# Optimization experiments

Measured on AMD Instinct MI355X. Metric: run time of the kernel, lower is better.

The kernel has to match this reference:

```python
import jax, jax.numpy as jnp
import numpy as np

B, TQ, TK, D, DV = 8, 2048, 2048, 1024, 1024  # units == TK


def setup_inputs() -> dict:
    key = jax.random.key(0)
    kq, kk, kv, kb = jax.random.split(key, 4)
    q = jax.random.normal(kq, (B, TQ, D), dtype=jnp.float32)
    k = jax.random.normal(kk, (B, D, TK), dtype=jnp.float32)
    v = jax.random.normal(kv, (B, TK, DV), dtype=jnp.float32)
    b = 0.1 * jax.random.normal(kb, (TK,), dtype=jnp.float32)  # bias over key axis (units,)
    return {"q": q, "k": k, "v": v, "b": b}


def reference(q, k, v, b):
    # scores[b,i,j] = tanh(q_i . k_j + b_j)   -- additive-style biased dot scores
    scores = jnp.tanh(jnp.einsum("bqd,bdk->bqk", q, k) + b)  # [B, TQ, TK]
    # softmax over the key axis (axis=1 of the unbatched [TQ,TK] scores)
    weights = jax.nn.softmax(scores, axis=-1)
    # weighted sum of values
    context = jnp.einsum("bqk,bkv->bqv", weights, v)  # [B, TQ, DV]
    return context
```

## Files before the change

### kernel.cpp

```cpp
#include <hip/hip_runtime.h>
#include <hip/hip_bf16.h>
#include <stdint.h>

#define B_  8
#define TQ_ 2048
#define TK_ 2048
#define D_  1024
#define DV_ 1024

typedef __attribute__((ext_vector_type(8))) short  short8;
typedef __attribute__((ext_vector_type(4))) float  floatx4;

__device__ __forceinline__ void async_copy16(const void* g, void* l) {
  __builtin_amdgcn_global_load_lds(
      (const __attribute__((address_space(1))) unsigned int*)g,
      (__attribute__((address_space(3))) unsigned int*)l,
      16, 0, 0);
}

__device__ __forceinline__ ushort f2bf(float f) {
  union { __hip_bfloat16 b; ushort u; } cv;
  cv.b = __float2bfloat16(f);
  return cv.u;
}

__device__ __forceinline__ float bf2f(ushort u) {
  union { ushort u; __hip_bfloat16 b; } cv;
  cv.u = u;
  return __bfloat162float(cv.b);
}


__device__ __forceinline__ void transpose_body(const float* __restrict__ in,
                                               ushort* __restrict__ out,
                                               int R, int C, int r0, int c0,
                                               float (*tile)[65]) {
  const int t = threadIdx.x;
  {
    const int row = t >> 4, col = (t & 15) * 4;
    #pragma unroll
    for (int ro = 0; ro < 4; ro++) {
      const float4 f = *(const float4*)&in[(size_t)(r0 + ro * 16 + row) * C + c0 + col];
      tile[ro * 16 + row][col + 0] = f.x;
      tile[ro * 16 + row][col + 1] = f.y;
      tile[ro * 16 + row][col + 2] = f.z;
      tile[ro * 16 + row][col + 3] = f.w;
    }
  }
  __syncthreads();
  {
    const int c = t >> 4, rg = (t & 15) * 4;
    #pragma unroll
    for (int ro = 0; ro < 4; ro++) {
      const int cc = ro * 16 + c;
      ushort4 o;
      o.x = f2bf(tile[rg + 0][cc]);
      o.y = f2bf(tile[rg + 1][cc]);
      o.z = f2bf(tile[rg + 2][cc]);
      o.w = f2bf(tile[rg + 3][cc]);
      *(ushort4*)&out[(size_t)(c0 + cc) * R + r0 + rg] = o;
    }
  }
}

__global__ void prep(const float* __restrict__ q, const float* __restrict__ k,
                     const float* __restrict__ v, ushort* __restrict__ qb,
                     ushort* __restrict__ ktb, ushort* __restrict__ vtb) {
  __shared__ float tile[64][65];
  const int task = blockIdx.z >> 3;
  const int z    = blockIdx.z & 7;
  if (task == 0) {
    const float4* in  = (const float4*)(q + (size_t)z * TQ_ * D_);
    ushort4*      oup = (ushort4*)(qb + (size_t)z * TQ_ * D_);
    const int i0 = (blockIdx.y * 32 + blockIdx.x) * 1024 + threadIdx.x;
    #pragma unroll
    for (int it = 0; it < 4; it++) {
      const int i = i0 + it * 256;
      float4 f = in[i];
      ushort4 o;
      o.x = f2bf(f.x); o.y = f2bf(f.y); o.z = f2bf(f.z); o.w = f2bf(f.w);
      oup[i] = o;
    }
  } else if (task == 1) {
    transpose_body(k + (size_t)z * D_ * TK_, ktb + (size_t)z * TK_ * D_,
                   D_, TK_, blockIdx.y * 64, blockIdx.x * 64, tile);
  } else {
    transpose_body(v + (size_t)z * TK_ * DV_, vtb + (size_t)z * DV_ * TK_,
                   TK_, DV_, blockIdx.x * 64, blockIdx.y * 64, tile);
  }
}

template <int KDIM>
__device__ __forceinline__ void gemm_core(const ushort* __restrict__ Ab,
                                          const ushort* __restrict__ Bb,
                                          ushort* ldsA, ushort* ldsB,
                                          int bm0, int bn0,
                                          floatx4 (&acc)[4][4]) {
  const int t    = threadIdx.x;
  const int lane = t & 63;
  const int w    = t >> 6;
  const int wm   = w >> 1, wn = w & 1;
  const int lc   = lane & 15;
  const int q    = lane >> 4;

  const int achunk = (t & 3) ^ ((t >> 3) & 3);
  const char* ga0 = (const char*)(Ab + (size_t)(bm0 + (t >> 2)) * KDIM) + achunk * 16;
  const char* ga1 = ga0 + (size_t)64 * KDIM * 2;
  const char* gb0 = (const char*)(Bb + (size_t)(bn0 + (t >> 2)) * KDIM) + achunk * 16;
  const char* gb1 = gb0 + (size_t)64 * KDIM * 2;
  char* la0 = (char*)ldsA + t * 16;
  char* la1 = (char*)ldsA + 4096 + t * 16;
  char* lb0 = (char*)ldsB + t * 16;
  char* lb1 = (char*)ldsB + 4096 + t * 16;

  const int rA = wm * 64 + lc;
  const int rB = wn * 64 + lc;
  const int baseA = rA * 64 + (q ^ ((rA >> 1) & 3)) * 16;
  const int baseB = rB * 64 + (q ^ ((rB >> 1) & 3)) * 16;

  #pragma unroll
  for (int mi = 0; mi < 4; mi++)
    #pragma unroll
    for (int ni = 0; ni < 4; ni++)
      acc[mi][ni] = (floatx4){0.f, 0.f, 0.f, 0.f};

  async_copy16(ga0, la0);
  async_copy16(ga1, la1);
  async_copy16(gb0, lb0);
  async_copy16(gb1, lb1);
  ga0 += 64; ga1 += 64; gb0 += 64; gb1 += 64;

  int cur = 0;
  for (int k0 = 0; k0 < KDIM; k0 += 32) {
    __syncthreads();
    if (k0 + 32 < KDIM) {
      const int nxt = cur ^ 8192;
      async_copy16(ga0, la0 + nxt);
      async_copy16(ga1, la1 + nxt);
      async_copy16(gb0, lb0 + nxt);
      async_copy16(gb1, lb1 + nxt);
      ga0 += 64; ga1 += 64; gb0 += 64; gb1 += 64;
    }

    short8 af[4], bfr[4];
    #pragma unroll
    for (int i = 0; i < 4; i++)
      af[i]  = *(const short8*)((const char*)ldsA + cur + baseA + i * 1024);
    #pragma unroll
    for (int i = 0; i < 4; i++)
      bfr[i] = *(const short8*)((const char*)ldsB + cur + baseB + i * 1024);
    #pragma unroll
    for (int mi = 0; mi < 4; mi++)
      #pragma unroll
      for (int ni = 0; ni < 4; ni++)
        acc[mi][ni] = __builtin_amdgcn_mfma_f32_16x16x32_bf16(af[mi], bfr[ni],
                                                              acc[mi][ni], 0, 0, 0);
    cur ^= 8192;
  }
}

__global__ void gemm_qk(const ushort* __restrict__ Q, const ushort* __restrict__ Kt,
                        const float* __restrict__ bias, ushort* __restrict__ P,
                        float* __restrict__ lsum) {
  __shared__ ushort ldsA[2 * 128 * 32];
  __shared__ ushort ldsB[2 * 128 * 32];
  const int z   = blockIdx.z;
  const int bm0 = blockIdx.y * 128;
  const int bn0 = blockIdx.x * 128;

  floatx4 acc[4][4];
  gemm_core<D_>(Q + (size_t)z * TQ_ * D_, Kt + (size_t)z * TK_ * D_,
                ldsA, ldsB, bm0, bn0, acc);

  const int lane = threadIdx.x & 63;
  const int w    = threadIdx.x >> 6;
  const int wm   = w >> 1, wn = w & 1;
  const int lc   = lane & 15;
  ushort* Pb = P + (size_t)z * TQ_ * TK_;
  float*  lz = lsum + z * TQ_;

  #pragma unroll
  for (int mi = 0; mi < 4; mi++) {
    int grow = bm0 + wm * 64 + mi * 16 + ((lane >> 4) << 2);
    float rs[4] = {0.f, 0.f, 0.f, 0.f};
    #pragma unroll
    for (int ni = 0; ni < 4; ni++) {
      int gcol = bn0 + wn * 64 + ni * 16 + lc;
      float bj = bias[gcol];
      #pragma unroll
      for (int r = 0; r < 4; r++) {
        float s = acc[mi][ni][r] + bj;
        float tnh = 1.f - 2.f / (__expf(2.f * s) + 1.f);
        float p   = __expf(tnh);
        ushort pu = f2bf(p);
        Pb[(size_t)(grow + r) * TK_ + gcol] = pu;
        rs[r] += bf2f(pu);
      }
    }
    #pragma unroll
    for (int r = 0; r < 4; r++) {
      rs[r] += __shfl_xor(rs[r], 1, 64);
      rs[r] += __shfl_xor(rs[r], 2, 64);
      rs[r] += __shfl_xor(rs[r], 4, 64);
      rs[r] += __shfl_xor(rs[r], 8, 64);
    }
    if (lc == 0) {
      #pragma unroll
      for (int r = 0; r < 4; r++) atomicAdd(&lz[grow + r], rs[r]);
    }
  }
}

__global__ void gemm_pv(const ushort* __restrict__ P, const ushort* __restrict__ Vt,
                        const float* __restrict__ lsum, float* __restrict__ out) {
  __shared__ ushort ldsA[2 * 128 * 32];
  __shared__ ushort ldsB[2 * 128 * 32];
  const int z   = blockIdx.z;
  const int bm0 = blockIdx.y * 128;
  const int bn0 = blockIdx.x * 128;

  floatx4 acc[4][4];
  gemm_core<TK_>(P + (size_t)z * TQ_ * TK_, Vt + (size_t)z * DV_ * TK_,
                 ldsA, ldsB, bm0, bn0, acc);

  const int lane = threadIdx.x & 63;
  const int w    = threadIdx.x >> 6;
  const int wm   = w >> 1, wn = w & 1;
  const int lc   = lane & 15;
  float* ob = out + (size_t)z * TQ_ * DV_;
  const float* lz = lsum + z * TQ_;

  #pragma unroll
  for (int mi = 0; mi < 4; mi++) {
    int grow = bm0 + wm * 64 + mi * 16 + ((lane >> 4) << 2);
    float linv[4];
    #pragma unroll
    for (int r = 0; r < 4; r++) linv[r] = 1.f / lz[grow + r];
    #pragma unroll
    for (int ni = 0; ni < 4; ni++) {
      int gcol = bn0 + wn * 64 + ni * 16 + lc;
      #pragma unroll
      for (int r = 0; r < 4; r++)
        ob[(size_t)(grow + r) * DV_ + gcol] = acc[mi][ni][r] * linv[r];
    }
  }
}


extern "C" void kernel_launch(void* const* d_in, const int* in_sizes, int n_in,
                              void* d_out, int out_size, void* d_ws, size_t ws_size,
                              hipStream_t stream) {
  const float* q    = (const float*)d_in[0];
  const float* k    = (const float*)d_in[1];
  const float* v    = (const float*)d_in[2];
  const float* bias = (const float*)d_in[3];
  float* out = (float*)d_out;

  char* ws = (char*)d_ws;
  ushort* qb   = (ushort*)(ws);
  ushort* ktb  = (ushort*)(ws + 33554432);
  ushort* vtb  = (ushort*)(ws + 67108864);
  ushort* P    = (ushort*)(ws + 100663296);
  float*  lsum = (float*)(ws + 167772160);

  hipMemsetAsync(lsum, 0, B_ * TQ_ * sizeof(float), stream);

  prep<<<dim3(32, 16, 24), dim3(256), 0, stream>>>(q, k, v, qb, ktb, vtb);

  gemm_qk<<<dim3(TK_ / 128, TQ_ / 128, B_), dim3(256), 0, stream>>>(qb, ktb, bias, P, lsum);
  gemm_pv<<<dim3(DV_ / 128, TQ_ / 128, B_), dim3(256), 0, stream>>>(P, vtb, lsum, out);
}
```

Baseline: 412.0 us.

## Enlarge GEMM tiles to 256x256 with 8 waves and ping-pong LDS pipeline

Replaces the 128x128, 4-wave GEMM core with a 256x256-tile, 8-wave core. Each K step is 64 wide and double-buffered in a 128KB LDS region. The A and B stages are staggered and issued with explicit vmcnt waits, and MFMA phases are split into quadrants raised with s_setprio. This raises arithmetic intensity per tile and overlaps global-to-LDS loads with compute. The cost is many more workgroup barriers, heavier register use (32 accumulators per thread), and fewer blocks, which may hurt occupancy and tail balance for the smaller PV GEMM.

```diff
diff --git a/kernel.cpp b/kernel.cpp
--- a/kernel.cpp
+++ b/kernel.cpp
@@ -90,105 +90,177 @@
   }
 }
 
+
+#define WG_BARRIER() do { asm volatile("" ::: "memory");        \
+                          __builtin_amdgcn_s_barrier();         \
+                          asm volatile("" ::: "memory"); } while (0)
+#define VMCNT(n) asm volatile("s_waitcnt vmcnt(" #n ")" ::: "memory")
+
+__device__ __forceinline__ void stage128(const ushort* __restrict__ gp, int grow0,
+                                         int k0, int KD, char* lds, int t) {
+  const int rr  = t >> 3;
+  const int s   = t & 7;
+  const int gch = s ^ (rr & 7);
+  const char* g0 = (const char*)(gp + (size_t)(grow0 + rr) * KD + k0) + gch * 16;
+  async_copy16(g0, lds + t * 16);
+  const char* g1 = (const char*)(gp + (size_t)(grow0 + 64 + rr) * KD + k0) + gch * 16;
+  async_copy16(g1, lds + 8192 + t * 16);
+}
+
+template <int MH>
+__device__ __forceinline__ void loadA(short8 (&a)[4][2], const char* Ab,
+                                      int rowA, int off0, int off1) {
+  #pragma unroll
+  for (int j = 0; j < 4; ++j) {
+    const char* p = Ab + rowA + (MH * 4 + j) * 2048;
+    a[j][0] = *(const short8*)(p + off0);
+    a[j][1] = *(const short8*)(p + off1);
+  }
+}
+
+template <int NH>
+__device__ __forceinline__ void loadB(short8 (&b)[2][2], const char* Bb,
+                                      int rowB, int off0, int off1) {
+  #pragma unroll
+  for (int i = 0; i < 2; ++i) {
+    const char* p = Bb + rowB + (NH * 2 + i) * 2048;
+    b[i][0] = *(const short8*)(p + off0);
+    b[i][1] = *(const short8*)(p + off1);
+  }
+}
+
+template <int MH, int NH>
+__device__ __forceinline__ void qmfma(floatx4 (&acc)[8][4], const short8 (&a)[4][2],
+                                      const short8 (&b)[2][2]) {
+  #pragma unroll
+  for (int j = 0; j < 4; ++j)
+    #pragma unroll
+    for (int i = 0; i < 2; ++i) {
+      floatx4 c = acc[MH * 4 + j][NH * 2 + i];
+      c = __builtin_amdgcn_mfma_f32_16x16x32_bf16(a[j][0], b[i][0], c, 0, 0, 0);
+      c = __builtin_amdgcn_mfma_f32_16x16x32_bf16(a[j][1], b[i][1], c, 0, 0, 0);
+      acc[MH * 4 + j][NH * 2 + i] = c;
+    }
+}
+
 template <int KDIM>
-__device__ __forceinline__ void gemm_core(const ushort* __restrict__ Ab,
-                                          const ushort* __restrict__ Bb,
-                                          ushort* ldsA, ushort* ldsB,
-                                          int bm0, int bn0,
-                                          floatx4 (&acc)[4][4]) {
+__device__ __forceinline__ void gemm_core8(const ushort* __restrict__ Ap,
+                                           const ushort* __restrict__ Bp,
+                                           char* lds, int bm0, int bn0,
+                                           floatx4 (&acc)[8][4]) {
   const int t    = threadIdx.x;
   const int lane = t & 63;
   const int w    = t >> 6;
-  const int wm   = w >> 1, wn = w & 1;
-  const int lc   = lane & 15;
-  const int q    = lane >> 4;
-
-  const int achunk = (t & 3) ^ ((t >> 3) & 3);
-  const char* ga0 = (const char*)(Ab + (size_t)(bm0 + (t >> 2)) * KDIM) + achunk * 16;
-  const char* ga1 = ga0 + (size_t)64 * KDIM * 2;
-  const char* gb0 = (const char*)(Bb + (size_t)(bn0 + (t >> 2)) * KDIM) + achunk * 16;
-  const char* gb1 = gb0 + (size_t)64 * KDIM * 2;
-  char* la0 = (char*)ldsA + t * 16;
-  char* la1 = (char*)ldsA + 4096 + t * 16;
-  char* lb0 = (char*)ldsB + t * 16;
-  char* lb1 = (char*)ldsB + 4096 + t * 16;
-
-  const int rA = wm * 64 + lc;
-  const int rB = wn * 64 + lc;
-  const int baseA = rA * 64 + (q ^ ((rA >> 1) & 3)) * 16;
-  const int baseB = rB * 64 + (q ^ ((rB >> 1) & 3)) * 16;
-
-  #pragma unroll
-  for (int mi = 0; mi < 4; mi++)
-    #pragma unroll
-    for (int ni = 0; ni < 4; ni++)
+  const int wm   = w >> 2, wn = w & 3;
+  const int lc   = lane & 15, q = lane >> 4;
+  const int sw   = lc & 7;
+  const int off0 = ((q)     ^ sw) * 16;
+  const int off1 = ((4 + q) ^ sw) * 16;
+  const int rowA = (wm * 128 + lc) * 128;
+  const int rowB = (wn * 64  + lc) * 128;
+  constexpr int NT = KDIM / 64;
+
+  #pragma unroll
+  for (int mi = 0; mi < 8; ++mi)
+    #pragma unroll
+    for (int ni = 0; ni < 4; ++ni)
       acc[mi][ni] = (floatx4){0.f, 0.f, 0.f, 0.f};
 
-  async_copy16(ga0, la0);
-  async_copy16(ga1, la1);
-  async_copy16(gb0, lb0);
-  async_copy16(gb1, lb1);
-  ga0 += 64; ga1 += 64; gb0 += 64; gb1 += 64;
-
-  int cur = 0;
-  for (int k0 = 0; k0 < KDIM; k0 += 32) {
-    __syncthreads();
-    if (k0 + 32 < KDIM) {
-      const int nxt = cur ^ 8192;
-      async_copy16(ga0, la0 + nxt);
-      async_copy16(ga1, la1 + nxt);
-      async_copy16(gb0, lb0 + nxt);
-      async_copy16(gb1, lb1 + nxt);
-      ga0 += 64; ga1 += 64; gb0 += 64; gb1 += 64;
-    }
-
-    short8 af[4], bfr[4];
-    #pragma unroll
-    for (int i = 0; i < 4; i++)
-      af[i]  = *(const short8*)((const char*)ldsA + cur + baseA + i * 1024);
-    #pragma unroll
-    for (int i = 0; i < 4; i++)
-      bfr[i] = *(const short8*)((const char*)ldsB + cur + baseB + i * 1024);
-    #pragma unroll
-    for (int mi = 0; mi < 4; mi++)
-      #pragma unroll
-      for (int ni = 0; ni < 4; ni++)
-        acc[mi][ni] = __builtin_amdgcn_mfma_f32_16x16x32_bf16(af[mi], bfr[ni],
-                                                              acc[mi][ni], 0, 0, 0);
-    cur ^= 8192;
-  }
-}
-
-__global__ void gemm_qk(const ushort* __restrict__ Q, const ushort* __restrict__ Kt,
-                        const float* __restrict__ bias, ushort* __restrict__ P,
-                        float* __restrict__ lsum) {
-  __shared__ ushort ldsA[2 * 128 * 32];
-  __shared__ ushort ldsB[2 * 128 * 32];
+  char* A0b = lds;
+  char* A1b = lds + 32768;
+  char* B0b = lds + 65536;
+
+  stage128(Ap, bm0,       0,  KDIM, A0b,         t);
+  stage128(Ap, bm0 + 128, 0,  KDIM, A0b + 16384, t);
+  stage128(Bp, bn0,       0,  KDIM, B0b,         t);
+  stage128(Bp, bn0 + 128, 0,  KDIM, B0b + 16384, t);
+  stage128(Ap, bm0,       64, KDIM, A1b,         t);
+  stage128(Ap, bm0 + 128, 64, KDIM, A1b + 16384, t);
+  VMCNT(4);
+  WG_BARRIER();
+
+  short8 a[4][2], b[2][2];
+  #pragma unroll 2
+  for (int tt = 0; tt < NT; ++tt) {
+    char* Ab = lds + (tt & 1) * 32768;
+    char* Bb = lds + 65536 + (tt & 1) * 32768;
+    char* Bn = lds + 65536 + ((tt + 1) & 1) * 32768;
+
+    loadA<0>(a, Ab, rowA, off0, off1);
+    loadB<0>(b, Bb, rowB, off0, off1);
+    if (tt + 1 < NT) {
+      const int kb = (tt + 1) * 64;
+      stage128(Bp, bn0,       kb, KDIM, Bn,         t);
+      stage128(Bp, bn0 + 128, kb, KDIM, Bn + 16384, t);
+    }
+    WG_BARRIER();
+    __builtin_amdgcn_s_setprio(1);
+    qmfma<0, 0>(acc, a, b);
+    __builtin_amdgcn_s_setprio(0);
+    WG_BARRIER();
+
+    loadB<1>(b, Bb, rowB, off0, off1);
+    WG_BARRIER();
+    __builtin_amdgcn_s_setprio(1);
+    qmfma<0, 1>(acc, a, b);
+    __builtin_amdgcn_s_setprio(0);
+    WG_BARRIER();
+
+    loadA<1>(a, Ab, rowA, off0, off1);
+    WG_BARRIER();
+    __builtin_amdgcn_s_setprio(1);
+    qmfma<1, 1>(acc, a, b);
+    __builtin_amdgcn_s_setprio(0);
+    WG_BARRIER();
+
+    loadB<0>(b, Bb, rowB, off0, off1);
+    if (tt + 2 < NT) {
+      const int ka = (tt + 2) * 64;
+      stage128(Ap, bm0,       ka, KDIM, Ab,         t);
+      stage128(Ap, bm0 + 128, ka, KDIM, Ab + 16384, t);
+      VMCNT(4);
+    } else {
+      VMCNT(0);
+    }
+    WG_BARRIER();
+    __builtin_amdgcn_s_setprio(1);
+    qmfma<1, 0>(acc, a, b);
+    __builtin_amdgcn_s_setprio(0);
+    WG_BARRIER();
+  }
+}
+
+__global__ __launch_bounds__(512, 2)
+void gemm_qk(const ushort* __restrict__ Q, const ushort* __restrict__ Kt,
+             const float* __restrict__ bias, ushort* __restrict__ P,
+             float* __restrict__ lsum) {
+  __shared__ short8 ldsv[8192];
+  char* lds = (char*)ldsv;
   const int z   = blockIdx.z;
-  const int bm0 = blockIdx.y * 128;
-  const int bn0 = blockIdx.x * 128;
-
-  floatx4 acc[4][4];
-  gemm_core<D_>(Q + (size_t)z * TQ_ * D_, Kt + (size_t)z * TK_ * D_,
-                ldsA, ldsB, bm0, bn0, acc);
+  const int bm0 = blockIdx.y * 256;
+  const int bn0 = blockIdx.x * 256;
+
+  floatx4 acc[8][4];
+  gemm_core8<D_>(Q + (size_t)z * TQ_ * D_, Kt + (size_t)z * TK_ * D_,
+                 lds, bm0, bn0, acc);
 
   const int lane = threadIdx.x & 63;
   const int w    = threadIdx.x >> 6;
-  const int wm   = w >> 1, wn = w & 1;
-  const int lc   = lane & 15;
+  const int wm   = w >> 2, wn = w & 3;
+  const int lc   = lane & 15, q = lane >> 4;
   ushort* Pb = P + (size_t)z * TQ_ * TK_;
   float*  lz = lsum + z * TQ_;
 
   #pragma unroll
-  for (int mi = 0; mi < 4; mi++) {
-    int grow = bm0 + wm * 64 + mi * 16 + ((lane >> 4) << 2);
+  for (int mi = 0; mi < 8; ++mi) {
+    const int grow = bm0 + wm * 128 + mi * 16 + (q << 2);
     float rs[4] = {0.f, 0.f, 0.f, 0.f};
     #pragma unroll
-    for (int ni = 0; ni < 4; ni++) {
-      int gcol = bn0 + wn * 64 + ni * 16 + lc;
-      float bj = bias[gcol];
+    for (int ni = 0; ni < 4; ++ni) {
+      const int gcol = bn0 + wn * 64 + ni * 16 + lc;
+      const float bj = bias[gcol];
       #pragma unroll
-      for (int r = 0; r < 4; r++) {
+      for (int r = 0; r < 4; ++r) {
         float s = acc[mi][ni][r] + bj;
         float tnh = 1.f - 2.f / (__expf(2.f * s) + 1.f);
         float p   = __expf(tnh);
@@ -198,7 +270,7 @@
       }
     }
     #pragma unroll
-    for (int r = 0; r < 4; r++) {
+    for (int r = 0; r < 4; ++r) {
       rs[r] += __shfl_xor(rs[r], 1, 64);
       rs[r] += __shfl_xor(rs[r], 2, 64);
       rs[r] += __shfl_xor(rs[r], 4, 64);
@@ -206,41 +278,42 @@
     }
     if (lc == 0) {
       #pragma unroll
-      for (int r = 0; r < 4; r++) atomicAdd(&lz[grow + r], rs[r]);
-    }
-  }
-}
-
-__global__ void gemm_pv(const ushort* __restrict__ P, const ushort* __restrict__ Vt,
-                        const float* __restrict__ lsum, float* __restrict__ out) {
-  __shared__ ushort ldsA[2 * 128 * 32];
-  __shared__ ushort ldsB[2 * 128 * 32];
+      for (int r = 0; r < 4; ++r) atomicAdd(&lz[grow + r], rs[r]);
+    }
+  }
+}
+
+__global__ __launch_bounds__(512, 2)
+void gemm_pv(const ushort* __restrict__ P, const ushort* __restrict__ Vt,
+             const float* __restrict__ lsum, float* __restrict__ out) {
+  __shared__ short8 ldsv[8192];
+  char* lds = (char*)ldsv;
   const int z   = blockIdx.z;
-  const int bm0 = blockIdx.y * 128;
-  const int bn0 = blockIdx.x * 128;
-
-  floatx4 acc[4][4];
-  gemm_core<TK_>(P + (size_t)z * TQ_ * TK_, Vt + (size_t)z * DV_ * TK_,
-                 ldsA, ldsB, bm0, bn0, acc);
+  const int bm0 = blockIdx.y * 256;
+  const int bn0 = blockIdx.x * 256;
+
+  floatx4 acc[8][4];
+  gemm_core8<TK_>(P + (size_t)z * TQ_ * TK_, Vt + (size_t)z * DV_ * TK_,
+                  lds, bm0, bn0, acc);
 
   const int lane = threadIdx.x & 63;
   const int w    = threadIdx.x >> 6;
-  const int wm   = w >> 1, wn = w & 1;
-  const int lc   = lane & 15;
+  const int wm   = w >> 2, wn = w & 3;
+  const int lc   = lane & 15, q = lane >> 4;
   float* ob = out + (size_t)z * TQ_ * DV_;
   const float* lz = lsum + z * TQ_;
 
   #pragma unroll
-  for (int mi = 0; mi < 4; mi++) {
-    int grow = bm0 + wm * 64 + mi * 16 + ((lane >> 4) << 2);
+  for (int mi = 0; mi < 8; ++mi) {
+    const int grow = bm0 + wm * 128 + mi * 16 + (q << 2);
     float linv[4];
     #pragma unroll
-    for (int r = 0; r < 4; r++) linv[r] = 1.f / lz[grow + r];
-    #pragma unroll
-    for (int ni = 0; ni < 4; ni++) {
-      int gcol = bn0 + wn * 64 + ni * 16 + lc;
+    for (int r = 0; r < 4; ++r) linv[r] = 1.f / lz[grow + r];
+    #pragma unroll
+    for (int ni = 0; ni < 4; ++ni) {
+      const int gcol = bn0 + wn * 64 + ni * 16 + lc;
       #pragma unroll
-      for (int r = 0; r < 4; r++)
+      for (int r = 0; r < 4; ++r)
         ob[(size_t)(grow + r) * DV_ + gcol] = acc[mi][ni][r] * linv[r];
     }
   }
@@ -267,6 +340,6 @@
 
   prep<<<dim3(32, 16, 24), dim3(256), 0, stream>>>(q, k, v, qb, ktb, vtb);
 
-  gemm_qk<<<dim3(TK_ / 128, TQ_ / 128, B_), dim3(256), 0, stream>>>(qb, ktb, bias, P, lsum);
-  gemm_pv<<<dim3(DV_ / 128, TQ_ / 128, B_), dim3(256), 0, stream>>>(P, vtb, lsum, out);
-}
+  gemm_qk<<<dim3(TK_ / 256, TQ_ / 256, B_), dim3(512), 0, stream>>>(qb, ktb, bias, P, lsum);
+  gemm_pv<<<dim3(DV_ / 256, TQ_ / 256, B_), dim3(512), 0, stream>>>(P, vtb, lsum, out);
+}
```

Result: faster. 379.1 us (-8.0%).
